# Kernel optimization log

Measured on AMD Instinct MI355X. Metric: run time of the kernel, lower is better.

Reference implementation:

```python
import jax, jax.numpy as jnp
import numpy as np

B = 64        # decode batch (num_tokens)
S = 2048      # max_kv_len
H = 2048      # hidden_size
HQ = 16       # num query heads
HKV = 4       # num kv heads
D = 128       # head_dim
RD = 64       # rope_dim = head_dim * 0.5
P = B * S     # kv pool size
EPS = 1e-6
SCALE = D ** -0.5


def rms_norm(x, w):
    xf = x.astype(jnp.float32)
    var = jnp.mean(xf * xf, axis=-1, keepdims=True)
    return (w.astype(jnp.float32) * (xf * jax.lax.rsqrt(var + EPS))).astype(x.dtype)


def rotate_half(x):
    x1, x2 = x[..., : x.shape[-1] // 2], x[..., x.shape[-1] // 2:]
    return jnp.concatenate([-x2, x1], axis=-1)


def apply_rope(x, cos, sin):
    # x: [T, heads, D]; cos/sin: [T, 1, RD]; partial rotary on first RD dims
    x_rot, x_pass = x[..., :RD], x[..., RD:]
    x_emb = x_rot * cos + rotate_half(x_rot) * sin
    return jnp.concatenate([x_emb, x_pass], axis=-1)


def setup_inputs() -> dict:
    key = jax.random.key(0)
    ks = jax.random.split(key, 10)
    f32 = jnp.float32
    hidden_states = jax.random.normal(ks[0], (B, H), f32)
    Wq = jax.random.normal(ks[1], (HQ * D, H), f32) * 0.02
    Wk = jax.random.normal(ks[2], (HKV * D, H), f32) * 0.02
    Wv = jax.random.normal(ks[3], (HKV * D, H), f32) * 0.02
    Wo = jax.random.normal(ks[4], (H, HQ * D), f32) * 0.02
    q_norm_w = jnp.ones((D,), f32)
    k_norm_w = jnp.ones((D,), f32)
    key_cache = jax.random.normal(ks[5], (P, HKV, D), f32)
    value_cache = jax.random.normal(ks[6], (P, HKV, D), f32)
    seq_lens = jax.random.randint(ks[7], (B,), S // 2, S + 1).astype(jnp.int32)
    req_pool_indices = jnp.arange(B, dtype=jnp.int32)
    req_to_token = jnp.arange(P, dtype=jnp.int32).reshape(B, S)
    out_cache_loc = (req_pool_indices * S + (seq_lens - 1)).astype(jnp.int32)
    # RoPE tables for the current decode positions (seq_len - 1)
    pos = (seq_lens - 1).astype(f32)
    inv_freq = 1.0 / (10000.0 ** (jnp.arange(0, RD, 2, dtype=f32) / RD))  # [RD/2]
    ang = pos[:, None] * inv_freq[None, :]                                 # [B, RD/2]
    cos = jnp.concatenate([jnp.cos(ang), jnp.cos(ang)], axis=-1)           # [B, RD]
    sin = jnp.concatenate([jnp.sin(ang), jnp.sin(ang)], axis=-1)
    return dict(hidden_states=hidden_states, Wq=Wq, Wk=Wk, Wv=Wv,
                q_norm_w=q_norm_w, k_norm_w=k_norm_w, Wo=Wo,
                key_cache=key_cache, value_cache=value_cache, cos=cos, sin=sin,
                req_to_token=req_to_token, req_pool_indices=req_pool_indices,
                seq_lens=seq_lens, out_cache_loc=out_cache_loc)


def reference(hidden_states, Wq, Wk, Wv, q_norm_w, k_norm_w, Wo,
              key_cache, value_cache, cos, sin,
              req_to_token, req_pool_indices, seq_lens, out_cache_loc):
    G = HQ // HKV  # GQA groups
    # fused qkv projection
    q = (hidden_states @ Wq.T).reshape(B, HQ, D)
    k = (hidden_states @ Wk.T).reshape(B, HKV, D)
    v = (hidden_states @ Wv.T).reshape(B, HKV, D)
    # per-head RMSNorm
    q = rms_norm(q, q_norm_w)
    k = rms_norm(k, k_norm_w)
    # partial rotary embedding (sliding_attention layer -> rope applied)
    q = apply_rope(q, cos[:, None, :], sin[:, None, :])
    k = apply_rope(k, cos[:, None, :], sin[:, None, :])
    # write new token K/V into the paged pool
    key_cache = key_cache.at[out_cache_loc].set(k)
    value_cache = value_cache.at[out_cache_loc].set(v)
    # paged gather: [B, S, HKV, D]
    token_indices = req_to_token[req_pool_indices]
    k_pad = key_cache[token_indices].transpose(0, 2, 1, 3)    # [B, HKV, S, D]
    v_pad = value_cache[token_indices].transpose(0, 2, 1, 3)  # [B, HKV, S, D]
    # padding mask over kv positions
    mask = jnp.arange(S)[None, :] < seq_lens[:, None]          # [B, S]
    # attention (q_len = 1 per request), grouped-query
    qg = q.reshape(B, HKV, G, D)
    scores = jnp.einsum('bkgd,bksd->bkgs', qg, k_pad) * SCALE  # [B, HKV, G, S]
    scores = jnp.where(mask[:, None, None, :], scores, jnp.finfo(scores.dtype).min)
    attn = jax.nn.softmax(scores, axis=-1)
    out = jnp.einsum('bkgs,bksd->bkgd', attn, v_pad).reshape(B, HQ * D)
    return out @ Wo.T
```

## Files before the change

kernel.cpp:

```cpp
#include <hip/hip_runtime.h>
#include <math.h>

#define BB 64
#define SS 2048
#define HH 2048
#define HQ 16
#define HKV 4
#define DD 128
#define RD 64
#define GG 4
#define QKV_N 3072
#define SCALE 0.08838834764831845f
#define QKSPLIT 8
#define OSPLIT 16
#define NSPLIT 8
#define CHUNK 256

__device__ __forceinline__ void gemm_tile(const float* __restrict__ A,
                                          const float* __restrict__ W,
                                          float* __restrict__ Cpart,
                                          int ldC, int colbase, int wrow0,
                                          int k0, int krange) {
  __shared__ __align__(16) float As[32][68];
  __shared__ __align__(16) float Ws[32][132];
  const int tid = threadIdx.x;
  const int tm = tid >> 4, tn = tid & 15;
  float acc[4][8] = {};
  const int kend = k0 + krange;

  float4 areg[2], wreg[4];
  #pragma unroll
  for (int q = 0; q < 2; q++) {
    const int p = tid + q * 256, mm = p >> 3, cc = p & 7;
    areg[q] = *(const float4*)(A + (size_t)mm * HH + k0 + cc * 4);
  }
  #pragma unroll
  for (int q = 0; q < 4; q++) {
    const int p = tid + q * 256, rr = p >> 3, cc = p & 7;
    wreg[q] = *(const float4*)(W + (size_t)(wrow0 + rr) * HH + k0 + cc * 4);
  }

  for (int kk = k0; kk < kend; kk += 32) {
    #pragma unroll
    for (int q = 0; q < 2; q++) {
      const int p = tid + q * 256, mm = p >> 3, cc = p & 7;
      As[cc*4+0][mm] = areg[q].x; As[cc*4+1][mm] = areg[q].y;
      As[cc*4+2][mm] = areg[q].z; As[cc*4+3][mm] = areg[q].w;
    }
    #pragma unroll
    for (int q = 0; q < 4; q++) {
      const int p = tid + q * 256, rr = p >> 3, cc = p & 7;
      Ws[cc*4+0][rr] = wreg[q].x; Ws[cc*4+1][rr] = wreg[q].y;
      Ws[cc*4+2][rr] = wreg[q].z; Ws[cc*4+3][rr] = wreg[q].w;
    }
    __syncthreads();
    if (kk + 32 < kend) {
      #pragma unroll
      for (int q = 0; q < 2; q++) {
        const int p = tid + q * 256, mm = p >> 3, cc = p & 7;
        areg[q] = *(const float4*)(A + (size_t)mm * HH + kk + 32 + cc * 4);
      }
      #pragma unroll
      for (int q = 0; q < 4; q++) {
        const int p = tid + q * 256, rr = p >> 3, cc = p & 7;
        wreg[q] = *(const float4*)(W + (size_t)(wrow0 + rr) * HH + kk + 32 + cc * 4);
      }
    }
    #pragma unroll
    for (int k = 0; k < 32; k++) {
      const float4 av  = *(const float4*)&As[k][tm * 4];
      const float4 wv0 = *(const float4*)&Ws[k][tn * 8];
      const float4 wv1 = *(const float4*)&Ws[k][tn * 8 + 4];
      const float a4[4] = {av.x, av.y, av.z, av.w};
      const float w8[8] = {wv0.x, wv0.y, wv0.z, wv0.w, wv1.x, wv1.y, wv1.z, wv1.w};
      #pragma unroll
      for (int i = 0; i < 4; i++)
        #pragma unroll
        for (int j = 0; j < 8; j++)
          acc[i][j] += a4[i] * w8[j];
    }
    __syncthreads();
  }
  #pragma unroll
  for (int i = 0; i < 4; i++) {
    float* dst = Cpart + (size_t)(tm*4 + i) * ldC + colbase + tn*8;
    *(float4*)dst       = make_float4(acc[i][0], acc[i][1], acc[i][2], acc[i][3]);
    *(float4*)(dst + 4) = make_float4(acc[i][4], acc[i][5], acc[i][6], acc[i][7]);
  }
}

__global__ __launch_bounds__(256) void maple_gemm_qkv(const float* __restrict__ A,
                                                      const float* __restrict__ Wq,
                                                      const float* __restrict__ Wk,
                                                      const float* __restrict__ Wv,
                                                      float* __restrict__ qkv_part) {
  const int col0 = blockIdx.x * 128;
  const int ks = blockIdx.y;
  const float* W; int wrow0;
  if (col0 < 2048)      { W = Wq; wrow0 = col0; }
  else if (col0 < 2560) { W = Wk; wrow0 = col0 - 2048; }
  else                  { W = Wv; wrow0 = col0 - 2560; }
  gemm_tile(A, W, qkv_part + (size_t)ks * BB * QKV_N, QKV_N, col0, wrow0,
            ks * (HH / QKSPLIT), HH / QKSPLIT);
}

__global__ __launch_bounds__(256) void maple_gemm_o(const float* __restrict__ A,
                                                    const float* __restrict__ W,
                                                    float* __restrict__ out_part) {
  const int col0 = blockIdx.x * 128;
  const int ks = blockIdx.y;
  gemm_tile(A, W, out_part + (size_t)ks * BB * HH, HH, col0, col0,
            ks * (HH / OSPLIT), HH / OSPLIT);
}

__global__ __launch_bounds__(128) void maple_norm_rope(const float* __restrict__ qkv_part,
                                                       const float* __restrict__ qw,
                                                       const float* __restrict__ kw,
                                                       const float* __restrict__ cosb,
                                                       const float* __restrict__ sinb,
                                                       float* __restrict__ qbuf,
                                                       float* __restrict__ kbuf,
                                                       float* __restrict__ vbuf) {
  const int h = blockIdx.x;
  const int b = blockIdx.y;
  const int tid = threadIdx.x;
  __shared__ float xs[128];
  __shared__ float red[2];
  int col; const float* w;
  if (h < HQ) { col = h * DD + tid;                w = qw; }
  else        { col = 2048 + (h - HQ) * DD + tid;  w = kw; }
  float x = 0.0f;
  #pragma unroll
  for (int ks = 0; ks < QKSPLIT; ks++)
    x += qkv_part[(size_t)ks * BB * QKV_N + (size_t)b * QKV_N + col];
  if (h >= HQ) {
    float xv = 0.0f;
    #pragma unroll
    for (int ks = 0; ks < QKSPLIT; ks++)
      xv += qkv_part[(size_t)ks * BB * QKV_N + (size_t)b * QKV_N + 2560 + (h - HQ) * DD + tid];
    vbuf[((size_t)b * HKV + (h - HQ)) * DD + tid] = xv;
  }
  float ss = x * x;
  #pragma unroll
  for (int off = 1; off < 64; off <<= 1) ss += __shfl_xor(ss, off);
  if ((tid & 63) == 0) red[tid >> 6] = ss;
  __syncthreads();
  const float var = (red[0] + red[1]) * (1.0f / 128.0f);
  const float r = rsqrtf(var + 1e-6f);
  const float xn = w[tid] * x * r;
  xs[tid] = xn;
  __syncthreads();
  float o;
  if (tid < 32)      o = xn * cosb[b*RD + tid] - xs[tid + 32] * sinb[b*RD + tid];
  else if (tid < 64) o = xn * cosb[b*RD + tid] + xs[tid - 32] * sinb[b*RD + tid];
  else               o = xn;
  if (h < HQ) qbuf[((size_t)b * HQ  + h)        * DD + tid] = o;
  else        kbuf[((size_t)b * HKV + (h - HQ)) * DD + tid] = o;
}

__global__ __launch_bounds__(256) void maple_attn_split(const float* __restrict__ qbuf,
                                                        const float* __restrict__ kbuf,
                                                        const float* __restrict__ vbuf,
                                                        const float* __restrict__ kc,
                                                        const float* __restrict__ vc,
                                                        const int* __restrict__ req_to_token,
                                                        const int* __restrict__ rpi,
                                                        const int* __restrict__ seq_lens,
                                                        float* __restrict__ part,
                                                        float* __restrict__ part_l) {
  const int c  = blockIdx.x;
  const int kh = blockIdx.y;
  const int b  = blockIdx.z;
  const int L  = seq_lens[b];
  const int s0 = c * CHUNK;
  if (s0 >= L) return;
  const int tid = threadIdx.x;
  const int w = tid >> 6, lane = tid & 63, tsub = lane >> 4, dsub = lane & 15;
  const int last = L - 1;
  const int s1 = min(s0 + CHUNK, L);

  __shared__ float qs[GG * DD];
  for (int i = tid; i < GG * DD; i += 256)
    qs[i] = qbuf[((size_t)b * HQ + kh * GG) * DD + i] * SCALE;
  __syncthreads();

  float qf[GG][8];
  #pragma unroll
  for (int g = 0; g < GG; g++)
    #pragma unroll
    for (int j = 0; j < 8; j++) qf[g][j] = qs[g * DD + dsub * 8 + j];

  float l[GG] = {0,0,0,0}, acc[GG][8] = {};
  const int* trow = req_to_token + (size_t)rpi[b] * SS;
  const size_t fresh = ((size_t)b * HKV + kh) * DD + dsub * 8;

  for (int s = s0 + w * 4; s < s1; s += 16) {
    const int t = s + tsub;
    const bool valid = (t < s1);
    const int tt = valid ? t : s0;
    float4 k0, k1, v0, v1;
    if (tt == last) {
      k0 = *(const float4*)(kbuf + fresh); k1 = *(const float4*)(kbuf + fresh + 4);
      v0 = *(const float4*)(vbuf + fresh); v1 = *(const float4*)(vbuf + fresh + 4);
    } else {
      const int ci = trow[tt];
      const size_t base = ((size_t)ci * HKV + kh) * DD + dsub * 8;
      k0 = *(const float4*)(kc + base); k1 = *(const float4*)(kc + base + 4);
      v0 = *(const float4*)(vc + base); v1 = *(const float4*)(vc + base + 4);
    }
    float sc[GG];
    #pragma unroll
    for (int g = 0; g < GG; g++) {
      sc[g] = qf[g][0]*k0.x + qf[g][1]*k0.y + qf[g][2]*k0.z + qf[g][3]*k0.w
            + qf[g][4]*k1.x + qf[g][5]*k1.y + qf[g][6]*k1.z + qf[g][7]*k1.w;
    }
    #pragma unroll
    for (int off = 1; off < 16; off <<= 1) {
      #pragma unroll
      for (int g = 0; g < GG; g++) sc[g] += __shfl_xor(sc[g], off);
    }
    #pragma unroll
    for (int g = 0; g < GG; g++) {
      const float p = valid ? __expf(sc[g]) : 0.0f;
      l[g] += p;
      acc[g][0] += p*v0.x; acc[g][1] += p*v0.y; acc[g][2] += p*v0.z; acc[g][3] += p*v0.w;
      acc[g][4] += p*v1.x; acc[g][5] += p*v1.y; acc[g][6] += p*v1.z; acc[g][7] += p*v1.w;
    }
  }

  #pragma unroll
  for (int g = 0; g < GG; g++) {
    l[g] += __shfl_xor(l[g], 16);
    l[g] += __shfl_xor(l[g], 32);
    #pragma unroll
    for (int j = 0; j < 8; j++) {
      acc[g][j] += __shfl_xor(acc[g][j], 16);
      acc[g][j] += __shfl_xor(acc[g][j], 32);
    }
  }

  __shared__ float wacc[4][GG][DD];
  __shared__ float wl[4][GG];
  if (lane < 16) {
    #pragma unroll
    for (int g = 0; g < GG; g++)
      #pragma unroll
      for (int j = 0; j < 8; j++) wacc[w][g][lane * 8 + j] = acc[g][j];
  }
  if (lane == 0) {
    #pragma unroll
    for (int g = 0; g < GG; g++) wl[w][g] = l[g];
  }
  __syncthreads();

  const size_t pbase = ((size_t)b * HKV + kh) * NSPLIT + c;
  for (int i = tid; i < GG * DD; i += 256) {
    const int g = i >> 7, d = i & 127;
    part[pbase * (GG * DD) + i] =
        wacc[0][g][d] + wacc[1][g][d] + wacc[2][g][d] + wacc[3][g][d];
  }
  if (tid < GG)
    part_l[pbase * GG + tid] = wl[0][tid] + wl[1][tid] + wl[2][tid] + wl[3][tid];
}

__global__ __launch_bounds__(256) void maple_attn_combine(const float* __restrict__ part,
                                                          const float* __restrict__ part_l,
                                                          const int* __restrict__ seq_lens,
                                                          float* __restrict__ attn_out) {
  const int kh = blockIdx.x;
  const int b  = blockIdx.y;
  const int tid = threadIdx.x;
  const int nc = (seq_lens[b] + CHUNK - 1) / CHUNK;
  const size_t pb = ((size_t)b * HKV + kh) * NSPLIT;
  for (int i = tid; i < GG * DD; i += 256) {
    const int g = i >> 7, d = i & 127;
    float o = 0.0f, Ls = 0.0f;
    for (int c = 0; c < nc; c++) {
      o  += part[(pb + c) * (GG * DD) + i];
      Ls += part_l[(pb + c) * GG + g];
    }
    attn_out[((size_t)b * HQ + kh * GG + g) * DD + d] = o / Ls;
  }
}

__global__ __launch_bounds__(256) void maple_reduce_out(const float* __restrict__ out_part,
                                                        float* __restrict__ out) {
  const int i = blockIdx.x * 256 + threadIdx.x;
  float s = 0.0f;
  #pragma unroll
  for (int ks = 0; ks < OSPLIT; ks++)
    s += out_part[(size_t)ks * (BB * HH) + i];
  out[i] = s;
}

extern "C" void kernel_launch(void* const* d_in, const int* in_sizes, int n_in,
                              void* d_out, int out_size, void* d_ws, size_t ws_size,
                              hipStream_t stream) {
  const float* hidden = (const float*)d_in[0];
  const float* Wq     = (const float*)d_in[1];
  const float* Wk     = (const float*)d_in[2];
  const float* Wv     = (const float*)d_in[3];
  const float* qnw    = (const float*)d_in[4];
  const float* knw    = (const float*)d_in[5];
  const float* Wo     = (const float*)d_in[6];
  const float* key_cache   = (const float*)d_in[7];
  const float* value_cache = (const float*)d_in[8];
  const float* cosb   = (const float*)d_in[9];
  const float* sinb   = (const float*)d_in[10];
  const int* req_to_token = (const int*)d_in[11];
  const int* rpi          = (const int*)d_in[12];
  const int* seq_lens     = (const int*)d_in[13];
  float* out = (float*)d_out;

  float* ws = (float*)d_ws;
  float* qkv_part = ws;
  float* out_part = qkv_part + 1572864;
  float* qbuf     = out_part + 2097152;
  float* kbuf     = qbuf + 131072;
  float* vbuf     = kbuf + 32768;
  float* attn_out = vbuf + 32768;
  float* part     = attn_out + 131072;
  float* part_l   = part + 1048576;

  maple_gemm_qkv<<<dim3(24, QKSPLIT), 256, 0, stream>>>(hidden, Wq, Wk, Wv, qkv_part);
  maple_norm_rope<<<dim3(HQ + HKV, BB), 128, 0, stream>>>(qkv_part, qnw, knw, cosb, sinb,
                                                          qbuf, kbuf, vbuf);
  maple_attn_split<<<dim3(NSPLIT, HKV, BB), 256, 0, stream>>>(qbuf, kbuf, vbuf,
                                                              key_cache, value_cache,
                                                              req_to_token, rpi, seq_lens,
                                                              part, part_l);
  maple_attn_combine<<<dim3(HKV, BB), 256, 0, stream>>>(part, part_l, seq_lens, attn_out);
  maple_gemm_o<<<dim3(16, OSPLIT), 256, 0, stream>>>(attn_out, Wo, out_part);
  maple_reduce_out<<<dim3(512), 256, 0, stream>>>(out_part, out);
}
```

Baseline: 583.3 us.

## Software-pipeline KV loads in attention, peel fresh token, vectorize combine and reduce

The attention split loop now prefetches the next iteration's K/V rows into registers while computing the current one, and the freshly written token is handled in a separate peeled step instead of a per-iteration branch. Query scaling moves into the norm/rope kernel, so the attention kernel reads q straight from global memory with no shared-memory staging or barrier. The combine and output-reduce kernels switch to float4 loads and stores with fewer threads and blocks. This targets memory latency in the bandwidth-bound KV scan, at the cost of more live registers per thread, which may reduce occupancy.

```diff
diff --git a/kernel.cpp b/kernel.cpp
--- a/kernel.cpp
+++ b/kernel.cpp
@@ -154,7 +154,7 @@
   if (tid < 32)      o = xn * cosb[b*RD + tid] - xs[tid + 32] * sinb[b*RD + tid];
   else if (tid < 64) o = xn * cosb[b*RD + tid] + xs[tid - 32] * sinb[b*RD + tid];
   else               o = xn;
-  if (h < HQ) qbuf[((size_t)b * HQ  + h)        * DD + tid] = o;
+  if (h < HQ) qbuf[((size_t)b * HQ  + h)        * DD + tid] = o * SCALE;
   else        kbuf[((size_t)b * HKV + (h - HQ)) * DD + tid] = o;
 }
 
@@ -178,36 +178,78 @@
   const int w = tid >> 6, lane = tid & 63, tsub = lane >> 4, dsub = lane & 15;
   const int last = L - 1;
   const int s1 = min(s0 + CHUNK, L);
-
-  __shared__ float qs[GG * DD];
-  for (int i = tid; i < GG * DD; i += 256)
-    qs[i] = qbuf[((size_t)b * HQ + kh * GG) * DD + i] * SCALE;
-  __syncthreads();
+  const int e  = min(s1, last);
 
   float qf[GG][8];
-  #pragma unroll
-  for (int g = 0; g < GG; g++)
-    #pragma unroll
-    for (int j = 0; j < 8; j++) qf[g][j] = qs[g * DD + dsub * 8 + j];
+  const float* qb = qbuf + ((size_t)b * HQ + kh * GG) * DD + dsub * 8;
+  #pragma unroll
+  for (int g = 0; g < GG; g++) {
+    const float4 q0 = *(const float4*)(qb + g * DD);
+    const float4 q1 = *(const float4*)(qb + g * DD + 4);
+    qf[g][0]=q0.x; qf[g][1]=q0.y; qf[g][2]=q0.z; qf[g][3]=q0.w;
+    qf[g][4]=q1.x; qf[g][5]=q1.y; qf[g][6]=q1.z; qf[g][7]=q1.w;
+  }
 
   float l[GG] = {0,0,0,0}, acc[GG][8] = {};
   const int* trow = req_to_token + (size_t)rpi[b] * SS;
-  const size_t fresh = ((size_t)b * HKV + kh) * DD + dsub * 8;
-
-  for (int s = s0 + w * 4; s < s1; s += 16) {
-    const int t = s + tsub;
-    const bool valid = (t < s1);
-    const int tt = valid ? t : s0;
-    float4 k0, k1, v0, v1;
-    if (tt == last) {
-      k0 = *(const float4*)(kbuf + fresh); k1 = *(const float4*)(kbuf + fresh + 4);
-      v0 = *(const float4*)(vbuf + fresh); v1 = *(const float4*)(vbuf + fresh + 4);
-    } else {
-      const int ci = trow[tt];
+
+  int s = s0 + w * 4;
+  if (s < e) {
+    int t0 = s + tsub;
+    bool va = (t0 < e);
+    {
+      const int ci = trow[va ? t0 : s0];
       const size_t base = ((size_t)ci * HKV + kh) * DD + dsub * 8;
-      k0 = *(const float4*)(kc + base); k1 = *(const float4*)(kc + base + 4);
-      v0 = *(const float4*)(vc + base); v1 = *(const float4*)(vc + base + 4);
-    }
+      float4 k0a = *(const float4*)(kc + base);
+      float4 k1a = *(const float4*)(kc + base + 4);
+      float4 v0a = *(const float4*)(vc + base);
+      float4 v1a = *(const float4*)(vc + base + 4);
+      while (s < e) {
+        const int sn = s + 16;
+        float4 k0b, k1b, v0b, v1b;
+        bool vb = false;
+        if (sn < e) {
+          const int tn = sn + tsub;
+          vb = (tn < e);
+          const int cin = trow[vb ? tn : s0];
+          const size_t bn = ((size_t)cin * HKV + kh) * DD + dsub * 8;
+          k0b = *(const float4*)(kc + bn);
+          k1b = *(const float4*)(kc + bn + 4);
+          v0b = *(const float4*)(vc + bn);
+          v1b = *(const float4*)(vc + bn + 4);
+        } else {
+          k0b = k1b = v0b = v1b = make_float4(0.f, 0.f, 0.f, 0.f);
+        }
+        float sc[GG];
+        #pragma unroll
+        for (int g = 0; g < GG; g++) {
+          sc[g] = qf[g][0]*k0a.x + qf[g][1]*k0a.y + qf[g][2]*k0a.z + qf[g][3]*k0a.w
+                + qf[g][4]*k1a.x + qf[g][5]*k1a.y + qf[g][6]*k1a.z + qf[g][7]*k1a.w;
+        }
+        #pragma unroll
+        for (int off = 1; off < 16; off <<= 1) {
+          #pragma unroll
+          for (int g = 0; g < GG; g++) sc[g] += __shfl_xor(sc[g], off);
+        }
+        #pragma unroll
+        for (int g = 0; g < GG; g++) {
+          const float p = va ? __expf(sc[g]) : 0.0f;
+          l[g] += p;
+          acc[g][0] += p*v0a.x; acc[g][1] += p*v0a.y; acc[g][2] += p*v0a.z; acc[g][3] += p*v0a.w;
+          acc[g][4] += p*v1a.x; acc[g][5] += p*v1a.y; acc[g][6] += p*v1a.z; acc[g][7] += p*v1a.w;
+        }
+        k0a = k0b; k1a = k1b; v0a = v0b; v1a = v1b; va = vb;
+        s = sn;
+      }
+    }
+  }
+
+  if (last < s0 + CHUNK && w == 0 && tsub == 0) {
+    const size_t fresh = ((size_t)b * HKV + kh) * DD + dsub * 8;
+    const float4 k0 = *(const float4*)(kbuf + fresh);
+    const float4 k1 = *(const float4*)(kbuf + fresh + 4);
+    const float4 v0 = *(const float4*)(vbuf + fresh);
+    const float4 v1 = *(const float4*)(vbuf + fresh + 4);
     float sc[GG];
     #pragma unroll
     for (int g = 0; g < GG; g++) {
@@ -221,7 +263,7 @@
     }
     #pragma unroll
     for (int g = 0; g < GG; g++) {
-      const float p = valid ? __expf(sc[g]) : 0.0f;
+      const float p = __expf(sc[g]);
       l[g] += p;
       acc[g][0] += p*v0.x; acc[g][1] += p*v0.y; acc[g][2] += p*v0.z; acc[g][3] += p*v0.w;
       acc[g][4] += p*v1.x; acc[g][5] += p*v1.y; acc[g][6] += p*v1.z; acc[g][7] += p*v1.w;
@@ -263,34 +305,38 @@
     part_l[pbase * GG + tid] = wl[0][tid] + wl[1][tid] + wl[2][tid] + wl[3][tid];
 }
 
-__global__ __launch_bounds__(256) void maple_attn_combine(const float* __restrict__ part,
+__global__ __launch_bounds__(128) void maple_attn_combine(const float* __restrict__ part,
                                                           const float* __restrict__ part_l,
                                                           const int* __restrict__ seq_lens,
                                                           float* __restrict__ attn_out) {
   const int kh = blockIdx.x;
   const int b  = blockIdx.y;
   const int tid = threadIdx.x;
+  const int g = tid >> 5;
   const int nc = (seq_lens[b] + CHUNK - 1) / CHUNK;
   const size_t pb = ((size_t)b * HKV + kh) * NSPLIT;
-  for (int i = tid; i < GG * DD; i += 256) {
-    const int g = i >> 7, d = i & 127;
-    float o = 0.0f, Ls = 0.0f;
-    for (int c = 0; c < nc; c++) {
-      o  += part[(pb + c) * (GG * DD) + i];
-      Ls += part_l[(pb + c) * GG + g];
-    }
-    attn_out[((size_t)b * HQ + kh * GG + g) * DD + d] = o / Ls;
-  }
+  float4 o = make_float4(0.f, 0.f, 0.f, 0.f);
+  float Ls = 0.0f;
+  for (int c = 0; c < nc; c++) {
+    const float4 p = *(const float4*)(part + (pb + c) * (GG * DD) + tid * 4);
+    o.x += p.x; o.y += p.y; o.z += p.z; o.w += p.w;
+    Ls += part_l[(pb + c) * GG + g];
+  }
+  const float r = 1.0f / Ls;
+  *(float4*)(attn_out + ((size_t)b * HQ + kh * GG) * DD + tid * 4) =
+      make_float4(o.x * r, o.y * r, o.z * r, o.w * r);
 }
 
 __global__ __launch_bounds__(256) void maple_reduce_out(const float* __restrict__ out_part,
                                                         float* __restrict__ out) {
-  const int i = blockIdx.x * 256 + threadIdx.x;
-  float s = 0.0f;
-  #pragma unroll
-  for (int ks = 0; ks < OSPLIT; ks++)
-    s += out_part[(size_t)ks * (BB * HH) + i];
-  out[i] = s;
+  const int i = (blockIdx.x * 256 + threadIdx.x) * 4;
+  float4 s = make_float4(0.f, 0.f, 0.f, 0.f);
+  #pragma unroll
+  for (int ks = 0; ks < OSPLIT; ks++) {
+    const float4 p = *(const float4*)(out_part + (size_t)ks * (BB * HH) + i);
+    s.x += p.x; s.y += p.y; s.z += p.z; s.w += p.w;
+  }
+  *(float4*)(out + i) = s;
 }
 
 extern "C" void kernel_launch(void* const* d_in, const int* in_sizes, int n_in,
@@ -329,7 +375,7 @@
                                                               key_cache, value_cache,
                                                               req_to_token, rpi, seq_lens,
                                                               part, part_l);
-  maple_attn_combine<<<dim3(HKV, BB), 256, 0, stream>>>(part, part_l, seq_lens, attn_out);
+  maple_attn_combine<<<dim3(HKV, BB), 128, 0, stream>>>(part, part_l, seq_lens, attn_out);
   maple_gemm_o<<<dim3(16, OSPLIT), 256, 0, stream>>>(attn_out, Wo, out_part);
-  maple_reduce_out<<<dim3(512), 256, 0, stream>>>(out_part, out);
-}
+  maple_reduce_out<<<dim3(128), 256, 0, stream>>>(out_part, out);
+}
```

Measured after the change: 582.2 us. Within noise of the previous version (-0.2%).
